# Performance work log

Hardware: AMD Instinct MI355X
Metric: run time of the kernel (lower is better)

Reference implementation:

```python
import jax, jax.numpy as jnp
import numpy as np

N, S, F, E, H, O, L, FE = 8, 1024, 64, 512, 8, 64, 6, 4
HD = E // H
FF = FE * E


def setup_inputs() -> dict:
    key = jax.random.key(0)
    ks = iter(jax.random.split(key, 40))
    def rn(shape, s=0.02):
        return jax.random.normal(next(ks), shape, jnp.float32) * s
    return {
        'x': jax.random.normal(next(ks), (N, F, S), jnp.float32),
        'W_first': rn((F, E)), 'b_first': jnp.zeros((E,), jnp.float32),
        'pos_emb': rn((S, E)),
        'Wq': rn((L, HD, HD)), 'bq': jnp.zeros((L, HD), jnp.float32),
        'Wk': rn((L, HD, HD)), 'bk': jnp.zeros((L, HD), jnp.float32),
        'Wv': rn((L, HD, HD)), 'bv': jnp.zeros((L, HD), jnp.float32),
        'Wo': rn((L, E, E)), 'bo': jnp.zeros((L, E), jnp.float32),
        'g1': jnp.ones((L, E), jnp.float32), 'be1': jnp.zeros((L, E), jnp.float32),
        'Wf1': rn((L, E, FF)), 'bf1': jnp.zeros((L, FF), jnp.float32),
        'Wf2': rn((L, FF, E)), 'bf2': jnp.zeros((L, E), jnp.float32),
        'g2': jnp.ones((L, E), jnp.float32), 'be2': jnp.zeros((L, E), jnp.float32),
        'Wfin': rn((E, O)), 'bfin': jnp.zeros((O,), jnp.float32),
    }


def layernorm(x, g, b, eps=1e-5):
    m = jnp.mean(x, axis=-1, keepdims=True)
    v = jnp.mean(jnp.square(x - m), axis=-1, keepdims=True)
    return (x - m) * jax.lax.rsqrt(v + eps) * g + b


def reference(x, W_first, b_first, pos_emb, Wq, bq, Wk, bk, Wv, bv, Wo, bo,
              g1, be1, Wf1, bf1, Wf2, bf2, g2, be2, Wfin, bfin):
    # x: (N, F, S) -> (N, S, F)
    h = jax.nn.relu(jnp.einsum('nfs,fe->nse', x, W_first) + b_first) + pos_emb[None]
    scale = E ** 0.5  # note: module scales by sqrt(embed_size), not sqrt(head_dim)
    for i in range(L):
        t = h.reshape(N, S, H, HD)
        q = jnp.einsum('nshd,de->nshe', t, Wq[i]) + bq[i]
        k = jnp.einsum('nshd,de->nshe', t, Wk[i]) + bk[i]
        v = jnp.einsum('nshd,de->nshe', t, Wv[i]) + bv[i]
        energy = jnp.einsum('nqhd,nkhd->nhqk', q, k)  # (N,H,S,S)
        att = jax.nn.softmax(energy / scale, axis=-1)
        o = jnp.einsum('nhqk,nkhd->nqhd', att, v).reshape(N, S, E)
        o = jnp.einsum('nse,ef->nsf', o, Wo[i]) + bo[i]
        hx = layernorm(o + h, g1[i], be1[i])
        ff = jax.nn.relu(jnp.einsum('nse,ef->nsf', hx, Wf1[i]) + bf1[i])
        ff = jnp.einsum('nsf,fe->nse', ff, Wf2[i]) + bf2[i]
        h = layernorm(ff + hx, g2[i], be2[i])
    # Conv1d kernel_size=1 == pointwise linear over channels; output (N, O, S)
    return jnp.einsum('nse,eo->nos', h, Wfin) + bfin[None, :, None]
```

## Files before the change

kernel.cpp:

```cpp
#include <hip/hip_runtime.h>
#include <hip/hip_bf16.h>
#include <math.h>

#define N_ 8
#define S_ 1024
#define F_ 64
#define E_ 512
#define H_ 8
#define O_ 64
#define L_ 6
#define HD_ 64
#define FF_ 2048
#define SCALE_ 0.044194173824159216f
#define LOG2E_ 1.4426950408889634f
#define QSCALE_ (SCALE_ * LOG2E_)

typedef unsigned short u16;
typedef __attribute__((ext_vector_type(4))) unsigned short u16x4;
typedef __attribute__((ext_vector_type(8))) unsigned short u16x8;
typedef __attribute__((ext_vector_type(8))) short short8;
typedef __attribute__((ext_vector_type(4))) float floatx4;

__device__ __forceinline__ u16 f2b(float f) {
    union { float f; unsigned u; } v; v.f = f;
    unsigned u = v.u;
    unsigned r = (u + 0x7FFFu + ((u >> 16) & 1u)) >> 16;
    return (u16)r;
}
__device__ __forceinline__ u16 f2b_fast(float f) {
    union { float f; unsigned u; } v; v.f = f;
    return (u16)((v.u + 0x8000u) >> 16);
}
__device__ __forceinline__ float b2f(u16 h) {
    union { unsigned u; float f; } v; v.u = ((unsigned)h) << 16;
    return v.f;
}

__device__ __forceinline__ void gload16(const u16* g, u16* l) {
    __builtin_amdgcn_global_load_lds(
        (const __attribute__((address_space(1))) void*)g,
        (__attribute__((address_space(3))) void*)l, 16, 0, 0);
}

__global__ __launch_bounds__(256) void first_mfma(
    const float* __restrict__ x, const u16* __restrict__ wt,
    const float* __restrict__ bf, const float* __restrict__ pe,
    u16* __restrict__ resb)
{
    __shared__ u16 a_s[128][72];
    int t = threadIdx.x;
    int w = t >> 6, lane = t & 63, quad = lane >> 4, c16 = lane & 15;
    int rowhalf = w >> 1, colhalf = w & 1;
    int col0 = blockIdx.x * 128;
    int row0 = blockIdx.y * 128;
    int n = row0 >> 10, s0 = row0 & 1023;

    const float* xb = x + (size_t)n * F_ * S_ + s0;
    #pragma unroll
    for (int i = 0; i < 8; i++) {
        int pos = (t + i * 256) * 4;
        int f = pos >> 7, sl = pos & 127;
        float4 v = *(const float4*)&xb[(size_t)f * S_ + sl];
        a_s[sl + 0][f] = f2b_fast(v.x);
        a_s[sl + 1][f] = f2b_fast(v.y);
        a_s[sl + 2][f] = f2b_fast(v.z);
        a_s[sl + 3][f] = f2b_fast(v.w);
    }
    __syncthreads();

    floatx4 acc[4][4];
    #pragma unroll
    for (int mt = 0; mt < 4; mt++)
        #pragma unroll
        for (int nt = 0; nt < 4; nt++) acc[mt][nt] = (floatx4){0.f, 0.f, 0.f, 0.f};

    #pragma unroll
    for (int ks = 0; ks < 2; ks++) {
        short8 af[4], bfr[4];
        #pragma unroll
        for (int mt = 0; mt < 4; mt++)
            af[mt] = *(const short8*)&a_s[rowhalf * 64 + mt * 16 + c16][ks * 32 + quad * 8];
        #pragma unroll
        for (int nt = 0; nt < 4; nt++)
            bfr[nt] = *(const short8*)&wt[(size_t)(col0 + colhalf * 64 + nt * 16 + c16) * F_
                                          + ks * 32 + quad * 8];
        #pragma unroll
        for (int mt = 0; mt < 4; mt++)
            #pragma unroll
            for (int nt = 0; nt < 4; nt++)
                acc[mt][nt] = __builtin_amdgcn_mfma_f32_16x16x32_bf16(
                    af[mt], bfr[nt], acc[mt][nt], 0, 0, 0);
    }

    #pragma unroll
    for (int nt = 0; nt < 4; nt++) {
        int col = col0 + colhalf * 64 + nt * 16 + c16;
        float bv = bf[col];
        #pragma unroll
        for (int mt = 0; mt < 4; mt++) {
            #pragma unroll
            for (int r = 0; r < 4; r++) {
                size_t row = (size_t)row0 + rowhalf * 64 + mt * 16 + quad * 4 + r;
                int s = (int)(row & 1023);
                float v = fmaxf(acc[mt][nt][r] + bv, 0.f) + pe[(size_t)s * E_ + col];
                resb[row * E_ + col] = f2b_fast(v);
            }
        }
    }
}

__global__ __launch_bounds__(256) void wprep(
    const float* __restrict__ W_first, const float* __restrict__ Wo,
    const float* __restrict__ Wf1, const float* __restrict__ Wf2,
    const float* __restrict__ Wfin,
    const float* __restrict__ Wq, const float* __restrict__ Wk,
    const float* __restrict__ Wv,
    u16* __restrict__ w1t, u16* __restrict__ wot, u16* __restrict__ wf1t,
    u16* __restrict__ wf2t, u16* __restrict__ wft,
    u16* __restrict__ wqt, u16* __restrict__ wkt, u16* __restrict__ wvt)
{
    int b = blockIdx.x;
    int t = threadIdx.x;
    __shared__ float tile[32][33];
    const float* W; u16* Wt; int K, Nc, bx, by;
    if (b < 32) {
        W = W_first; Wt = w1t; K = F_; Nc = E_; bx = b & 15; by = b >> 4;
    } else if (b < 32 + 1536) {
        int i = b - 32; int z = i >> 8; int r = i & 255;
        W = Wo + (size_t)z * E_ * E_; Wt = wot + (size_t)z * E_ * E_;
        K = E_; Nc = E_; bx = r & 15; by = r >> 4;
    } else if (b < 32 + 1536 + 6144) {
        int i = b - (32 + 1536); int z = i >> 10; int r = i & 1023;
        W = Wf1 + (size_t)z * E_ * FF_; Wt = wf1t + (size_t)z * E_ * FF_;
        K = E_; Nc = FF_; bx = r & 63; by = r >> 6;
    } else if (b < 32 + 1536 + 12288) {
        int i = b - (32 + 1536 + 6144); int z = i >> 10; int r = i & 1023;
        W = Wf2 + (size_t)z * FF_ * E_; Wt = wf2t + (size_t)z * FF_ * E_;
        K = FF_; Nc = E_; bx = r & 15; by = r >> 4;
    } else if (b < 32 + 1536 + 12288 + 32) {
        int r = b - (32 + 1536 + 12288);
        W = Wfin; Wt = wft; K = E_; Nc = O_; bx = r & 1; by = r >> 1;
    } else {
        int l = b - (32 + 1536 + 12288 + 32);
        size_t off = (size_t)l * HD_ * HD_;
        #pragma unroll
        for (int i = 0; i < 16; i++) {
            int idx = t + i * 256;
            int e = idx >> 6, d = idx & 63;
            wqt[off + idx] = f2b(Wq[off + d * HD_ + e]);
            wkt[off + idx] = f2b(Wk[off + d * HD_ + e]);
            wvt[off + idx] = f2b(Wv[off + d * HD_ + e]);
        }
        return;
    }
    #pragma unroll
    for (int i = 0; i < 4; i++) {
        int q = t + i * 256; int r = q >> 5, c = q & 31;
        tile[r][c] = W[(size_t)(by * 32 + r) * Nc + bx * 32 + c];
    }
    __syncthreads();
    #pragma unroll
    for (int i = 0; i < 4; i++) {
        int q = t + i * 256; int r = q >> 5, c = q & 31;
        Wt[(size_t)(bx * 32 + r) * K + by * 32 + c] = f2b(tile[c][r]);
    }
}

__global__ __launch_bounds__(256) void qkv_mfma(
    const u16* __restrict__ hb,
    const u16* __restrict__ wqt, const u16* __restrict__ wkt,
    const u16* __restrict__ wvt,
    const float* __restrict__ bq, const float* __restrict__ bk,
    const float* __restrict__ bvp,
    u16* __restrict__ qo, u16* __restrict__ ko, u16* __restrict__ vt)
{
    __shared__ u16 a_s[128 * 64];
    int t = threadIdx.x;
    int w = t >> 6, lane = t & 63, quad = lane >> 4, c16 = lane & 15;
    size_t row0 = (size_t)blockIdx.x * 128;

    #pragma unroll
    for (int i = 0; i < 4; i++) {
        int q = t + i * 256; int r = q >> 3, c = q & 7;
        *(u16x8*)&a_s[r * 64 + ((c ^ (r & 7)) * 8)] =
            *(const u16x8*)&hb[(row0 + r) * HD_ + c * 8];
    }
    __syncthreads();

    short8 af[2][2];
    #pragma unroll
    for (int mt = 0; mt < 2; mt++)
        #pragma unroll
        for (int ks = 0; ks < 2; ks++) {
            int r = w * 32 + mt * 16 + c16;
            af[mt][ks] = *(const short8*)&a_s[r * 64 + (((ks * 4 + quad) ^ (r & 7)) * 8)];
        }

    const u16* wts[2] = {wqt, wkt};
    const float* bs[2] = {bq, bk};
    u16* outs[2] = {qo, ko};
    #pragma unroll
    for (int m = 0; m < 2; m++) {
        short8 bfr[4][2];
        #pragma unroll
        for (int nt = 0; nt < 4; nt++)
            #pragma unroll
            for (int ks = 0; ks < 2; ks++)
                bfr[nt][ks] = *(const short8*)&wts[m][(nt * 16 + c16) * HD_ + ks * 32 + quad * 8];
        floatx4 acc[2][4];
        #pragma unroll
        for (int mt = 0; mt < 2; mt++)
            #pragma unroll
            for (int nt = 0; nt < 4; nt++) acc[mt][nt] = (floatx4){0.f, 0.f, 0.f, 0.f};
        #pragma unroll
        for (int ks = 0; ks < 2; ks++)
            #pragma unroll
            for (int mt = 0; mt < 2; mt++)
                #pragma unroll
                for (int nt = 0; nt < 4; nt++)
                    acc[mt][nt] = __builtin_amdgcn_mfma_f32_16x16x32_bf16(
                        af[mt][ks], bfr[nt][ks], acc[mt][nt], 0, 0, 0);
        float osc = (m == 0) ? QSCALE_ : 1.0f;
        #pragma unroll
        for (int nt = 0; nt < 4; nt++) {
            float bv_ = bs[m][nt * 16 + c16];
            #pragma unroll
            for (int mt = 0; mt < 2; mt++)
                #pragma unroll
                for (int r = 0; r < 4; r++)
                    outs[m][(row0 + w * 32 + mt * 16 + quad * 4 + r) * HD_ + nt * 16 + c16] =
                        f2b_fast((acc[mt][nt][r] + bv_) * osc);
        }
    }

    {
        short8 bfr[4][2];
        #pragma unroll
        for (int nt = 0; nt < 4; nt++)
            #pragma unroll
            for (int ks = 0; ks < 2; ks++)
                bfr[nt][ks] = *(const short8*)&wvt[(nt * 16 + c16) * HD_ + ks * 32 + quad * 8];
        floatx4 acc[2][4];
        #pragma unroll
        for (int mt = 0; mt < 2; mt++)
            #pragma unroll
            for (int nt = 0; nt < 4; nt++) acc[mt][nt] = (floatx4){0.f, 0.f, 0.f, 0.f};
        #pragma unroll
        for (int ks = 0; ks < 2; ks++)
            #pragma unroll
            for (int mt = 0; mt < 2; mt++)
                #pragma unroll
                for (int nt = 0; nt < 4; nt++)
                    acc[mt][nt] = __builtin_amdgcn_mfma_f32_16x16x32_bf16(
                        af[mt][ks], bfr[nt][ks], acc[mt][nt], 0, 0, 0);

        __syncthreads();
        u16* vt_s = a_s;
        #pragma unroll
        for (int nt = 0; nt < 4; nt++) {
            float bv_ = bvp[nt * 16 + c16];
            #pragma unroll
            for (int mt = 0; mt < 2; mt++)
                #pragma unroll
                for (int r = 0; r < 4; r++) {
                    int fr = w * 32 + mt * 16 + quad * 4 + r;
                    int h = fr & 7, sl = fr >> 3;
                    vt_s[((h * 64 + nt * 16 + c16) * 16) + sl] =
                        f2b_fast(acc[mt][nt][r] + bv_);
                }
        }
        __syncthreads();
        int sflat0 = (int)(row0 >> 3);
        int n = sflat0 >> 10, sbase = sflat0 & 1023;
        #pragma unroll
        for (int i = 0; i < 4; i++) {
            int u = t + i * 256;
            int h = u >> 7, rest = u & 127, d = rest >> 1, half = rest & 1;
            *(u16x8*)&vt[((size_t)((n * 8 + h) * 64 + d)) * (size_t)S_ + sbase + half * 8] =
                *(u16x8*)&vt_s[(h * 64 + d) * 16 + half * 8];
        }
    }
}

__global__ __launch_bounds__(256, 4) void attn_mfma(
    const u16* __restrict__ Q, const u16* __restrict__ K,
    const u16* __restrict__ Vt, u16* __restrict__ O)
{
    int bid0 = blockIdx.x;
    int bid = (bid0 & 7) * 128 + (bid0 >> 3);
    int qt = bid & 15, hh = (bid >> 4) & 7, n = bid >> 7;
    int t = threadIdx.x;
    int w = t >> 6, lane = t & 63, quad = lane >> 4, c16 = lane & 15;

    __shared__ u16 qp_s[64 * 64];
    __shared__ u16 k_s[2][64 * 64];
    __shared__ u16 vt_s[2][64 * 64];
    u16* p_s = qp_s + w * 16 * 64;

    const size_t qkbase = (size_t)n * S_ * E_ + hh * 64;
    const size_t vtbase = ((size_t)(n * H_ + hh) * 64) * (size_t)S_;

    int ar = t >> 3, act = t & 7;
    int acq = act * 8;
    int scw[2];
    #pragma unroll
    for (int i = 0; i < 2; i++) scw[i] = ((act ^ ((ar + i * 32) & 7)) * 8);

    #pragma unroll
    for (int i = 0; i < 2; i++) {
        int q = t + i * 256; int r = q >> 3, c = q & 7;
        *(u16x8*)&qp_s[r * 64 + ((c ^ (r & 7)) * 8)] =
            *(const u16x8*)&Q[qkbase + (size_t)(qt * 64 + r) * E_ + c * 8];
    }
    u16x8 pk[2], pv[2];
    #pragma unroll
    for (int i = 0; i < 2; i++) {
        pk[i] = *(const u16x8*)&K[qkbase + (size_t)(ar + i * 32) * E_ + acq];
        pv[i] = *(const u16x8*)&Vt[vtbase + (size_t)(ar + i * 32) * S_ + acq];
    }
    __syncthreads();

    short8 qf[2];
    #pragma unroll
    for (int ks = 0; ks < 2; ks++) {
        int r = w * 16 + c16;
        qf[ks] = *(const short8*)&qp_s[r * 64 + (((ks * 4 + quad) ^ (r & 7)) * 8)];
    }

    #pragma unroll
    for (int i = 0; i < 2; i++) {
        int r = ar + i * 32;
        *(u16x8*)&k_s[0][r * 64 + scw[i]] = pk[i];
        *(u16x8*)&vt_s[0][r * 64 + scw[i]] = pv[i];
    }
    __syncthreads();

    const short8 ones = {(short)0x3F80, (short)0x3F80, (short)0x3F80, (short)0x3F80,
                         (short)0x3F80, (short)0x3F80, (short)0x3F80, (short)0x3F80};

    floatx4 oaccT[4];
    floatx4 lacc = (floatx4){0.f, 0.f, 0.f, 0.f};
    #pragma unroll
    for (int mt = 0; mt < 4; mt++) oaccT[mt] = (floatx4){0.f, 0.f, 0.f, 0.f};

    for (int k0 = 0; k0 < S_; k0 += 64) {
        int cur = (k0 >> 6) & 1;
        const u16* ks_ = k_s[cur];
        const u16* vs_ = vt_s[cur];
        bool more = (k0 + 64 < S_);
        if (more) {
            #pragma unroll
            for (int i = 0; i < 2; i++) {
                pk[i] = *(const u16x8*)&K[qkbase + (size_t)(k0 + 64 + ar + i * 32) * E_ + acq];
                pv[i] = *(const u16x8*)&Vt[vtbase + (size_t)(ar + i * 32) * S_ + k0 + 64 + acq];
            }
        }

        floatx4 st[4];
        #pragma unroll
        for (int mt = 0; mt < 4; mt++) st[mt] = (floatx4){0.f, 0.f, 0.f, 0.f};
        __builtin_amdgcn_s_setprio(1);
        #pragma unroll
        for (int ks = 0; ks < 2; ks++) {
            short8 kf[4];
            #pragma unroll
            for (int mt = 0; mt < 4; mt++) {
                int r = mt * 16 + c16;
                kf[mt] = *(const short8*)&ks_[r * 64 + (((ks * 4 + quad) ^ (r & 7)) * 8)];
            }
            #pragma unroll
            for (int mt = 0; mt < 4; mt++)
                st[mt] = __builtin_amdgcn_mfma_f32_16x16x32_bf16(
                    kf[mt], qf[ks], st[mt], 0, 0, 0);
        }
        __builtin_amdgcn_s_setprio(0);

        #pragma unroll
        for (int mt = 0; mt < 4; mt++) {
            u16x4 h;
            #pragma unroll
            for (int r = 0; r < 4; r++) h[r] = f2b_fast(exp2f(st[mt][r]));
            *(u16x4*)&p_s[c16 * 64 + (((2 * mt + (quad >> 1)) ^ (c16 & 7)) * 8)
                          + (quad & 1) * 4] = h;
        }

        __builtin_amdgcn_s_setprio(1);
        #pragma unroll
        for (int ks = 0; ks < 2; ks++) {
            short8 pf = *(const short8*)&p_s[c16 * 64 + (((ks * 4 + quad) ^ (c16 & 7)) * 8)];
            short8 vf[4];
            #pragma unroll
            for (int mt = 0; mt < 4; mt++) {
                int r = mt * 16 + c16;
                vf[mt] = *(const short8*)&vs_[r * 64 + (((ks * 4 + quad) ^ (r & 7)) * 8)];
            }
            lacc = __builtin_amdgcn_mfma_f32_16x16x32_bf16(ones, pf, lacc, 0, 0, 0);
            #pragma unroll
            for (int mt = 0; mt < 4; mt++)
                oaccT[mt] = __builtin_amdgcn_mfma_f32_16x16x32_bf16(
                    vf[mt], pf, oaccT[mt], 0, 0, 0);
        }
        __builtin_amdgcn_s_setprio(0);

        if (more) {
            u16* kd = k_s[cur ^ 1];
            u16* vd = vt_s[cur ^ 1];
            #pragma unroll
            for (int i = 0; i < 2; i++) {
                int r = ar + i * 32;
                *(u16x8*)&kd[r * 64 + scw[i]] = pk[i];
                *(u16x8*)&vd[r * 64 + scw[i]] = pv[i];
            }
        }
        __syncthreads();
    }

    {
        float rl = 1.f / lacc[0];
        int s = qt * 64 + w * 16 + c16;
        size_t base = (size_t)(n * S_ + s) * E_ + hh * 64;
        #pragma unroll
        for (int mt = 0; mt < 4; mt++) {
            u16x4 h;
            #pragma unroll
            for (int r = 0; r < 4; r++) h[r] = f2b_fast(oaccT[mt][r] * rl);
            *(u16x4*)&O[base + mt * 16 + quad * 4] = h;
        }
    }
}

template <int MT, int NT, bool RELU, bool HASRES, bool OUTF32, bool OUTBF16>
__global__ __launch_bounds__(256, 2) void gemm_mfma(
    const u16* __restrict__ A, const u16* __restrict__ Bt,
    const float* __restrict__ bias, const u16* __restrict__ resid,
    float* __restrict__ outf, u16* __restrict__ outb, int M, int Nc, int K)
{
    constexpr int MFR = MT / 32;
    constexpr int NFR = NT / 32;
    constexpr int AI  = MT / 32;
    constexpr int BI  = NT / 32;
    __shared__ u16 a_s[MT * 64];
    __shared__ u16 b_s[NT * 64];

    int t = threadIdx.x;
    int w = t >> 6, lane = t & 63, quad = lane >> 4, c16 = lane & 15;
    int rw = w >> 1, cw = w & 1;

    int gx = gridDim.x;
    int nwg = gx * (int)gridDim.y;
    int lin = (int)blockIdx.y * gx + (int)blockIdx.x;
    int cpx = nwg >> 3;
    int id2 = (lin & 7) * cpx + (lin >> 3);
    int bx = id2 % gx, by = id2 / gx;

    size_t row0 = (size_t)by * MT;
    size_t col0 = (size_t)bx * NT;

    size_t aoff[AI]; int adst[AI];
    #pragma unroll
    for (int i = 0; i < AI; i++) {
        int p = t + i * 256;
        int r = p >> 3;
        int kc = (p & 7) ^ (r & 7);
        aoff[i] = (row0 + r) * (size_t)K + kc * 8;
        adst[i] = w * 512 + i * 2048;
    }
    size_t boff[BI]; int bdst[BI];
    #pragma unroll
    for (int i = 0; i < BI; i++) {
        int p = t + i * 256;
        int r = p >> 3;
        int kc = (p & 7) ^ (r & 7);
        boff[i] = (col0 + r) * (size_t)K + kc * 8;
        bdst[i] = w * 512 + i * 2048;
    }

    floatx4 acc[MFR][NFR];
    #pragma unroll
    for (int mt = 0; mt < MFR; mt++)
        #pragma unroll
        for (int nt = 0; nt < NFR; nt++) acc[mt][nt] = (floatx4){0.f, 0.f, 0.f, 0.f};

    for (int k0 = 0; k0 < K; k0 += 64) {
        #pragma unroll
        for (int i = 0; i < AI; i++) gload16(A + aoff[i] + k0, a_s + adst[i]);
        #pragma unroll
        for (int i = 0; i < BI; i++) gload16(Bt + boff[i] + k0, b_s + bdst[i]);
        __syncthreads();

        #pragma unroll
        for (int ks = 0; ks < 2; ks++) {
            short8 af[MFR], bfr[NFR];
            #pragma unroll
            for (int mt = 0; mt < MFR; mt++) {
                int r = rw * (MT / 2) + mt * 16 + c16;
                af[mt] = *(const short8*)&a_s[r * 64 + (((ks * 4 + quad) ^ (r & 7)) * 8)];
            }
            #pragma unroll
            for (int nt = 0; nt < NFR; nt++) {
                int r = cw * (NT / 2) + nt * 16 + c16;
                bfr[nt] = *(const short8*)&b_s[r * 64 + (((ks * 4 + quad) ^ (r & 7)) * 8)];
            }
            #pragma unroll
            for (int mt = 0; mt < MFR; mt++)
                #pragma unroll
                for (int nt = 0; nt < NFR; nt++)
                    acc[mt][nt] = __builtin_amdgcn_mfma_f32_16x16x32_bf16(
                        af[mt], bfr[nt], acc[mt][nt], 0, 0, 0);
        }
        __syncthreads();
    }

    #pragma unroll
    for (int nt = 0; nt < NFR; nt++) {
        int col = (int)col0 + cw * (NT / 2) + nt * 16 + c16;
        float bv = bias[col];
        #pragma unroll
        for (int mt = 0; mt < MFR; mt++) {
            size_t rowb = row0 + rw * (MT / 2) + mt * 16 + quad * 4;
            #pragma unroll
            for (int r = 0; r < 4; r++) {
                size_t row = rowb + r;
                float v = acc[mt][nt][r] + bv;
                if constexpr (HASRES) v += b2f(resid[row * Nc + col]);
                if constexpr (RELU) v = fmaxf(v, 0.f);
                if constexpr (OUTF32) outf[row * Nc + col] = v;
                if constexpr (OUTBF16) outb[row * Nc + col] = f2b_fast(v);
            }
        }
    }
}

__global__ __launch_bounds__(256) void layernorm_k(
    const float* __restrict__ in, const float* __restrict__ g,
    const float* __restrict__ bb, u16* __restrict__ outb)
{
    int row = blockIdx.x;
    int t = threadIdx.x;
    const float* x = in + (size_t)row * E_;
    float x0 = x[t], x1 = x[t + 256];
    float s = x0 + x1;
    #pragma unroll
    for (int off = 32; off; off >>= 1) s += __shfl_down(s, off, 64);
    __shared__ float red[4];
    int wid = t >> 6, lane = t & 63;
    if (lane == 0) red[wid] = s;
    __syncthreads();
    float m = (red[0] + red[1] + red[2] + red[3]) * (1.f / E_);
    float d0 = x0 - m, d1 = x1 - m;
    float sq = d0 * d0 + d1 * d1;
    #pragma unroll
    for (int off = 32; off; off >>= 1) sq += __shfl_down(sq, off, 64);
    __syncthreads();
    if (lane == 0) red[wid] = sq;
    __syncthreads();
    float var = (red[0] + red[1] + red[2] + red[3]) * (1.f / E_);
    float rstd = rsqrtf(var + 1e-5f);
    outb[(size_t)row * E_ + t] = f2b_fast(d0 * rstd * g[t] + bb[t]);
    outb[(size_t)row * E_ + t + 256] = f2b_fast(d1 * rstd * g[t + 256] + bb[t + 256]);
}

__global__ __launch_bounds__(256) void final_mfma(
    const u16* __restrict__ hb, const u16* __restrict__ wft,
    const float* __restrict__ bfin, float* __restrict__ outp)
{
    __shared__ u16 a_s[64][72];
    int t = threadIdx.x;
    int w = t >> 6, lane = t & 63, quad = lane >> 4, c16 = lane & 15;
    size_t row0 = (size_t)blockIdx.x * 64;

    floatx4 acc[4];
    #pragma unroll
    for (int nt = 0; nt < 4; nt++) acc[nt] = (floatx4){0.f, 0.f, 0.f, 0.f};

    int ar = t >> 3, acq = (t & 7) * 8;
    u16x8 pa[2];
    #pragma unroll
    for (int i = 0; i < 2; i++)
        pa[i] = *(const u16x8*)&hb[(row0 + ar + i * 32) * E_ + acq];

    for (int k0 = 0; k0 < E_; k0 += 64) {
        #pragma unroll
        for (int i = 0; i < 2; i++)
            *(u16x8*)&a_s[ar + i * 32][acq] = pa[i];
        __syncthreads();
        if (k0 + 64 < E_) {
            #pragma unroll
            for (int i = 0; i < 2; i++)
                pa[i] = *(const u16x8*)&hb[(row0 + ar + i * 32) * E_ + k0 + 64 + acq];
        }
        #pragma unroll
        for (int ks = 0; ks < 2; ks++) {
            short8 af = *(const short8*)&a_s[w * 16 + c16][ks * 32 + quad * 8];
            #pragma unroll
            for (int nt = 0; nt < 4; nt++) {
                short8 bf = *(const short8*)&wft[(nt * 16 + c16) * E_ + k0 + ks * 32 + quad * 8];
                acc[nt] = __builtin_amdgcn_mfma_f32_16x16x32_bf16(af, bf, acc[nt], 0, 0, 0);
            }
        }
        __syncthreads();
    }

    #pragma unroll
    for (int nt = 0; nt < 4; nt++) {
        int o = nt * 16 + c16;
        float bv = bfin[o];
        #pragma unroll
        for (int r = 0; r < 4; r++) {
            size_t row = row0 + w * 16 + quad * 4 + r;
            int n = (int)(row >> 10), s = (int)(row & 1023);
            outp[((size_t)(n * O_ + o)) * S_ + s] = acc[nt][r] + bv;
        }
    }
}

extern "C" void kernel_launch(void* const* d_in, const int* in_sizes, int n_in,
                              void* d_out, int out_size, void* d_ws, size_t ws_size,
                              hipStream_t stream)
{
    const float* x       = (const float*)d_in[0];
    const float* W_first = (const float*)d_in[1];
    const float* b_first = (const float*)d_in[2];
    const float* pos_emb = (const float*)d_in[3];
    const float* Wq      = (const float*)d_in[4];
    const float* bq      = (const float*)d_in[5];
    const float* Wk      = (const float*)d_in[6];
    const float* bk      = (const float*)d_in[7];
    const float* Wv      = (const float*)d_in[8];
    const float* bv      = (const float*)d_in[9];
    const float* Wo      = (const float*)d_in[10];
    const float* bo      = (const float*)d_in[11];
    const float* g1      = (const float*)d_in[12];
    const float* be1     = (const float*)d_in[13];
    const float* Wf1     = (const float*)d_in[14];
    const float* bf1     = (const float*)d_in[15];
    const float* Wf2     = (const float*)d_in[16];
    const float* bf2     = (const float*)d_in[17];
    const float* g2      = (const float*)d_in[18];
    const float* be2     = (const float*)d_in[19];
    const float* Wfin    = (const float*)d_in[20];
    const float* bfin    = (const float*)d_in[21];
    float* out = (float*)d_out;

    const size_t M4 = (size_t)N_ * S_ * E_;
    float* t1   = (float*)d_ws;
    u16*   resb = (u16*)(t1 + M4);
    u16*   qb   = resb + M4;
    u16*   kb   = qb + M4;
    u16*   vt   = kb + M4;
    u16*   ob   = vt + M4;
    u16*   ffb  = qb;
    u16*   wot  = ob + M4;
    u16*   wf1t = wot + (size_t)L_ * E_ * E_;
    u16*   wf2t = wf1t + (size_t)L_ * E_ * FF_;
    u16*   wqt  = wf2t + (size_t)L_ * FF_ * E_;
    u16*   wkt  = wqt + (size_t)L_ * HD_ * HD_;
    u16*   wvt  = wkt + (size_t)L_ * HD_ * HD_;
    u16*   wft  = wvt + (size_t)L_ * HD_ * HD_;
    u16*   w1t  = wft + (size_t)O_ * E_;

    const int rows = N_ * S_;

    wprep<<<32 + 1536 + 12288 + 32 + 6, 256, 0, stream>>>(
        W_first, Wo, Wf1, Wf2, Wfin, Wq, Wk, Wv,
        w1t, wot, wf1t, wf2t, wft, wqt, wkt, wvt);

    first_mfma<<<dim3(E_ / 128, rows / 128), 256, 0, stream>>>(
        x, w1t, b_first, pos_emb, resb);

    for (int i = 0; i < L_; i++) {
        qkv_mfma<<<512, 256, 0, stream>>>(
            resb, wqt + (size_t)i * HD_ * HD_, wkt + (size_t)i * HD_ * HD_,
            wvt + (size_t)i * HD_ * HD_, bq + i * HD_, bk + i * HD_, bv + i * HD_,
            qb, kb, vt);
        attn_mfma<<<1024, 256, 0, stream>>>(qb, kb, vt, ob);
        gemm_mfma<128, 64, false, true, true, false><<<dim3(E_ / 64, rows / 128), 256, 0, stream>>>(
            ob, wot + (size_t)i * E_ * E_, bo + i * E_, resb, t1, nullptr, rows, E_, E_);
        layernorm_k<<<rows, 256, 0, stream>>>(t1, g1 + i * E_, be1 + i * E_, resb);
        gemm_mfma<128, 128, true, false, false, true><<<dim3(FF_ / 128, rows / 128), 256, 0, stream>>>(
            resb, wf1t + (size_t)i * E_ * FF_, bf1 + i * FF_, nullptr, nullptr, ffb,
            rows, FF_, E_);
        gemm_mfma<128, 64, false, true, true, false><<<dim3(E_ / 64, rows / 128), 256, 0, stream>>>(
            ffb, wf2t + (size_t)i * FF_ * E_, bf2 + i * E_, resb, t1, nullptr,
            rows, E_, FF_);
        layernorm_k<<<rows, 256, 0, stream>>>(t1, g2 + i * E_, be2 + i * E_, resb);
    }

    final_mfma<<<rows / 64, 256, 0, stream>>>(resb, wft, bfin, out);
}
```

Measured before the change: 1.005 ms.

## Load attention K/V and QKV inputs directly from global memory, dropping LDS staging

The attention kernel no longer stages K and V^T tiles in double-buffered shared memory. Each wave now loads its MFMA fragments straight from global memory (through cache) every iteration, which removes the block-wide barriers and LDS traffic. The QKV projection kernel likewise reads its A fragments from global memory instead of going through LDS. The trade is that every one of the four waves re-reads the same K/V tile from L2, the loads are no longer prefetched ahead of use, and global access patterns become less coalesced. That exposes memory latency inside the loop.

```diff
diff --git a/kernel.cpp b/kernel.cpp
--- a/kernel.cpp
+++ b/kernel.cpp
@@ -174,27 +174,18 @@
     const float* __restrict__ bvp,
     u16* __restrict__ qo, u16* __restrict__ ko, u16* __restrict__ vt)
 {
-    __shared__ u16 a_s[128 * 64];
+    __shared__ u16 vt_s[128 * 64];
     int t = threadIdx.x;
     int w = t >> 6, lane = t & 63, quad = lane >> 4, c16 = lane & 15;
     size_t row0 = (size_t)blockIdx.x * 128;
 
-    #pragma unroll
-    for (int i = 0; i < 4; i++) {
-        int q = t + i * 256; int r = q >> 3, c = q & 7;
-        *(u16x8*)&a_s[r * 64 + ((c ^ (r & 7)) * 8)] =
-            *(const u16x8*)&hb[(row0 + r) * HD_ + c * 8];
-    }
-    __syncthreads();
-
     short8 af[2][2];
     #pragma unroll
     for (int mt = 0; mt < 2; mt++)
         #pragma unroll
-        for (int ks = 0; ks < 2; ks++) {
-            int r = w * 32 + mt * 16 + c16;
-            af[mt][ks] = *(const short8*)&a_s[r * 64 + (((ks * 4 + quad) ^ (r & 7)) * 8)];
-        }
+        for (int ks = 0; ks < 2; ks++)
+            af[mt][ks] = *(const short8*)&hb[(row0 + w * 32 + mt * 16 + c16) * HD_
+                                             + ks * 32 + quad * 8];
 
     const u16* wts[2] = {wqt, wkt};
     const float* bs[2] = {bq, bk};
@@ -254,8 +245,6 @@
                     acc[mt][nt] = __builtin_amdgcn_mfma_f32_16x16x32_bf16(
                         af[mt][ks], bfr[nt][ks], acc[mt][nt], 0, 0, 0);
 
-        __syncthreads();
-        u16* vt_s = a_s;
         #pragma unroll
         for (int nt = 0; nt < 4; nt++) {
             float bv_ = bvp[nt * 16 + c16];
@@ -292,48 +281,20 @@
     int t = threadIdx.x;
     int w = t >> 6, lane = t & 63, quad = lane >> 4, c16 = lane & 15;
 
-    __shared__ u16 qp_s[64 * 64];
-    __shared__ u16 k_s[2][64 * 64];
-    __shared__ u16 vt_s[2][64 * 64];
-    u16* p_s = qp_s + w * 16 * 64;
+    __shared__ u16 p_all[4 * 16 * 64];
+    u16* p_s = p_all + w * 16 * 64;
 
     const size_t qkbase = (size_t)n * S_ * E_ + hh * 64;
     const size_t vtbase = ((size_t)(n * H_ + hh) * 64) * (size_t)S_;
 
-    int ar = t >> 3, act = t & 7;
-    int acq = act * 8;
-    int scw[2];
-    #pragma unroll
-    for (int i = 0; i < 2; i++) scw[i] = ((act ^ ((ar + i * 32) & 7)) * 8);
-
-    #pragma unroll
-    for (int i = 0; i < 2; i++) {
-        int q = t + i * 256; int r = q >> 3, c = q & 7;
-        *(u16x8*)&qp_s[r * 64 + ((c ^ (r & 7)) * 8)] =
-            *(const u16x8*)&Q[qkbase + (size_t)(qt * 64 + r) * E_ + c * 8];
-    }
-    u16x8 pk[2], pv[2];
-    #pragma unroll
-    for (int i = 0; i < 2; i++) {
-        pk[i] = *(const u16x8*)&K[qkbase + (size_t)(ar + i * 32) * E_ + acq];
-        pv[i] = *(const u16x8*)&Vt[vtbase + (size_t)(ar + i * 32) * S_ + acq];
-    }
-    __syncthreads();
-
     short8 qf[2];
     #pragma unroll
-    for (int ks = 0; ks < 2; ks++) {
-        int r = w * 16 + c16;
-        qf[ks] = *(const short8*)&qp_s[r * 64 + (((ks * 4 + quad) ^ (r & 7)) * 8)];
-    }
-
-    #pragma unroll
-    for (int i = 0; i < 2; i++) {
-        int r = ar + i * 32;
-        *(u16x8*)&k_s[0][r * 64 + scw[i]] = pk[i];
-        *(u16x8*)&vt_s[0][r * 64 + scw[i]] = pv[i];
-    }
-    __syncthreads();
+    for (int ks = 0; ks < 2; ks++)
+        qf[ks] = *(const short8*)&Q[qkbase + (size_t)(qt * 64 + w * 16 + c16) * E_
+                                    + ks * 32 + quad * 8];
+
+    const u16* kp = K + qkbase + (size_t)c16 * E_ + quad * 8;
+    const u16* vp = Vt + vtbase + (size_t)c16 * S_ + quad * 8;
 
     const short8 ones = {(short)0x3F80, (short)0x3F80, (short)0x3F80, (short)0x3F80,
                          (short)0x3F80, (short)0x3F80, (short)0x3F80, (short)0x3F80};
@@ -344,36 +305,31 @@
     for (int mt = 0; mt < 4; mt++) oaccT[mt] = (floatx4){0.f, 0.f, 0.f, 0.f};
 
     for (int k0 = 0; k0 < S_; k0 += 64) {
-        int cur = (k0 >> 6) & 1;
-        const u16* ks_ = k_s[cur];
-        const u16* vs_ = vt_s[cur];
-        bool more = (k0 + 64 < S_);
-        if (more) {
-            #pragma unroll
-            for (int i = 0; i < 2; i++) {
-                pk[i] = *(const u16x8*)&K[qkbase + (size_t)(k0 + 64 + ar + i * 32) * E_ + acq];
-                pv[i] = *(const u16x8*)&Vt[vtbase + (size_t)(ar + i * 32) * S_ + k0 + 64 + acq];
-            }
-        }
+        short8 kf[2][4];
+        #pragma unroll
+        for (int ks = 0; ks < 2; ks++)
+            #pragma unroll
+            for (int mt = 0; mt < 4; mt++)
+                kf[ks][mt] = *(const short8*)&kp[(size_t)(k0 + mt * 16) * E_ + ks * 32];
 
         floatx4 st[4];
         #pragma unroll
         for (int mt = 0; mt < 4; mt++) st[mt] = (floatx4){0.f, 0.f, 0.f, 0.f};
         __builtin_amdgcn_s_setprio(1);
         #pragma unroll
-        for (int ks = 0; ks < 2; ks++) {
-            short8 kf[4];
-            #pragma unroll
-            for (int mt = 0; mt < 4; mt++) {
-                int r = mt * 16 + c16;
-                kf[mt] = *(const short8*)&ks_[r * 64 + (((ks * 4 + quad) ^ (r & 7)) * 8)];
-            }
+        for (int ks = 0; ks < 2; ks++)
             #pragma unroll
             for (int mt = 0; mt < 4; mt++)
                 st[mt] = __builtin_amdgcn_mfma_f32_16x16x32_bf16(
-                    kf[mt], qf[ks], st[mt], 0, 0, 0);
-        }
+                    kf[ks][mt], qf[ks], st[mt], 0, 0, 0);
         __builtin_amdgcn_s_setprio(0);
+
+        short8 vf[2][4];
+        #pragma unroll
+        for (int ks = 0; ks < 2; ks++)
+            #pragma unroll
+            for (int mt = 0; mt < 4; mt++)
+                vf[ks][mt] = *(const short8*)&vp[(size_t)(mt * 16) * S_ + k0 + ks * 32];
 
         #pragma unroll
         for (int mt = 0; mt < 4; mt++) {
@@ -388,31 +344,13 @@
         #pragma unroll
         for (int ks = 0; ks < 2; ks++) {
             short8 pf = *(const short8*)&p_s[c16 * 64 + (((ks * 4 + quad) ^ (c16 & 7)) * 8)];
-            short8 vf[4];
-            #pragma unroll
-            for (int mt = 0; mt < 4; mt++) {
-                int r = mt * 16 + c16;
-                vf[mt] = *(const short8*)&vs_[r * 64 + (((ks * 4 + quad) ^ (r & 7)) * 8)];
-            }
             lacc = __builtin_amdgcn_mfma_f32_16x16x32_bf16(ones, pf, lacc, 0, 0, 0);
             #pragma unroll
             for (int mt = 0; mt < 4; mt++)
                 oaccT[mt] = __builtin_amdgcn_mfma_f32_16x16x32_bf16(
-                    vf[mt], pf, oaccT[mt], 0, 0, 0);
+                    vf[ks][mt], pf, oaccT[mt], 0, 0, 0);
         }
         __builtin_amdgcn_s_setprio(0);
-
-        if (more) {
-            u16* kd = k_s[cur ^ 1];
-            u16* vd = vt_s[cur ^ 1];
-            #pragma unroll
-            for (int i = 0; i < 2; i++) {
-                int r = ar + i * 32;
-                *(u16x8*)&kd[r * 64 + scw[i]] = pk[i];
-                *(u16x8*)&vd[r * 64 + scw[i]] = pv[i];
-            }
-        }
-        __syncthreads();
     }
 
     {
```

Measured after the change: 1.461 ms. 45.4% more time.

## Double query tile per attention block, load QKV A-fragments directly, vectorize layernorm

Applied to the files above, without the earlier changes.

Attention blocks now cover 128 queries instead of 64, with each wave holding two 16-row query fragments. Every K/V tile loaded into shared memory is therefore reused across twice as many queries, and the grid is halved. The cost is more accumulator registers, so occupancy drops to 2 blocks per SM. The QKV kernel now reads A-fragments straight from global memory, skipping the LDS staging and one barrier, and layernorm uses float2 loads and packed bf16 stores.

```diff
diff --git a/kernel.cpp b/kernel.cpp
--- a/kernel.cpp
+++ b/kernel.cpp
@@ -174,27 +174,18 @@
     const float* __restrict__ bvp,
     u16* __restrict__ qo, u16* __restrict__ ko, u16* __restrict__ vt)
 {
-    __shared__ u16 a_s[128 * 64];
+    __shared__ u16 vt_s[128 * 64];
     int t = threadIdx.x;
     int w = t >> 6, lane = t & 63, quad = lane >> 4, c16 = lane & 15;
     size_t row0 = (size_t)blockIdx.x * 128;
 
-    #pragma unroll
-    for (int i = 0; i < 4; i++) {
-        int q = t + i * 256; int r = q >> 3, c = q & 7;
-        *(u16x8*)&a_s[r * 64 + ((c ^ (r & 7)) * 8)] =
-            *(const u16x8*)&hb[(row0 + r) * HD_ + c * 8];
-    }
-    __syncthreads();
-
     short8 af[2][2];
     #pragma unroll
     for (int mt = 0; mt < 2; mt++)
         #pragma unroll
-        for (int ks = 0; ks < 2; ks++) {
-            int r = w * 32 + mt * 16 + c16;
-            af[mt][ks] = *(const short8*)&a_s[r * 64 + (((ks * 4 + quad) ^ (r & 7)) * 8)];
-        }
+        for (int ks = 0; ks < 2; ks++)
+            af[mt][ks] = *(const short8*)&hb[(row0 + w * 32 + mt * 16 + c16) * HD_
+                                             + ks * 32 + quad * 8];
 
     const u16* wts[2] = {wqt, wkt};
     const float* bs[2] = {bq, bk};
@@ -254,8 +245,6 @@
                     acc[mt][nt] = __builtin_amdgcn_mfma_f32_16x16x32_bf16(
                         af[mt][ks], bfr[nt][ks], acc[mt][nt], 0, 0, 0);
 
-        __syncthreads();
-        u16* vt_s = a_s;
         #pragma unroll
         for (int nt = 0; nt < 4; nt++) {
             float bv_ = bvp[nt * 16 + c16];
@@ -282,20 +271,20 @@
     }
 }
 
-__global__ __launch_bounds__(256, 4) void attn_mfma(
+__global__ __launch_bounds__(256, 2) void attn_mfma(
     const u16* __restrict__ Q, const u16* __restrict__ K,
     const u16* __restrict__ Vt, u16* __restrict__ O)
 {
     int bid0 = blockIdx.x;
-    int bid = (bid0 & 7) * 128 + (bid0 >> 3);
-    int qt = bid & 15, hh = (bid >> 4) & 7, n = bid >> 7;
+    int bid = (bid0 & 7) * 64 + (bid0 >> 3);
+    int qt = bid & 7, hh = (bid >> 3) & 7, n = bid >> 6;
     int t = threadIdx.x;
     int w = t >> 6, lane = t & 63, quad = lane >> 4, c16 = lane & 15;
 
-    __shared__ u16 qp_s[64 * 64];
+    __shared__ u16 qp_s[128 * 64];
     __shared__ u16 k_s[2][64 * 64];
     __shared__ u16 vt_s[2][64 * 64];
-    u16* p_s = qp_s + w * 16 * 64;
+    u16* p_s = qp_s + w * 32 * 64;
 
     const size_t qkbase = (size_t)n * S_ * E_ + hh * 64;
     const size_t vtbase = ((size_t)(n * H_ + hh) * 64) * (size_t)S_;
@@ -307,10 +296,10 @@
     for (int i = 0; i < 2; i++) scw[i] = ((act ^ ((ar + i * 32) & 7)) * 8);
 
     #pragma unroll
-    for (int i = 0; i < 2; i++) {
+    for (int i = 0; i < 4; i++) {
         int q = t + i * 256; int r = q >> 3, c = q & 7;
         *(u16x8*)&qp_s[r * 64 + ((c ^ (r & 7)) * 8)] =
-            *(const u16x8*)&Q[qkbase + (size_t)(qt * 64 + r) * E_ + c * 8];
+            *(const u16x8*)&Q[qkbase + (size_t)(qt * 128 + r) * E_ + c * 8];
     }
     u16x8 pk[2], pv[2];
     #pragma unroll
@@ -320,12 +309,14 @@
     }
     __syncthreads();
 
-    short8 qf[2];
-    #pragma unroll
-    for (int ks = 0; ks < 2; ks++) {
-        int r = w * 16 + c16;
-        qf[ks] = *(const short8*)&qp_s[r * 64 + (((ks * 4 + quad) ^ (r & 7)) * 8)];
-    }
+    short8 qf[2][2];
+    #pragma unroll
+    for (int nq = 0; nq < 2; nq++)
+        #pragma unroll
+        for (int ks = 0; ks < 2; ks++) {
+            int r = w * 32 + nq * 16 + c16;
+            qf[nq][ks] = *(const short8*)&qp_s[r * 64 + (((ks * 4 + quad) ^ (r & 7)) * 8)];
+        }
 
     #pragma unroll
     for (int i = 0; i < 2; i++) {
@@ -338,10 +329,14 @@
     const short8 ones = {(short)0x3F80, (short)0x3F80, (short)0x3F80, (short)0x3F80,
                          (short)0x3F80, (short)0x3F80, (short)0x3F80, (short)0x3F80};
 
-    floatx4 oaccT[4];
-    floatx4 lacc = (floatx4){0.f, 0.f, 0.f, 0.f};
-    #pragma unroll
-    for (int mt = 0; mt < 4; mt++) oaccT[mt] = (floatx4){0.f, 0.f, 0.f, 0.f};
+    floatx4 oaccT[4][2];
+    floatx4 lacc[2];
+    #pragma unroll
+    for (int nq = 0; nq < 2; nq++) {
+        lacc[nq] = (floatx4){0.f, 0.f, 0.f, 0.f};
+        #pragma unroll
+        for (int mt = 0; mt < 4; mt++) oaccT[mt][nq] = (floatx4){0.f, 0.f, 0.f, 0.f};
+    }
 
     for (int k0 = 0; k0 < S_; k0 += 64) {
         int cur = (k0 >> 6) & 1;
@@ -356,9 +351,11 @@
             }
         }
 
-        floatx4 st[4];
-        #pragma unroll
-        for (int mt = 0; mt < 4; mt++) st[mt] = (floatx4){0.f, 0.f, 0.f, 0.f};
+        floatx4 st[4][2];
+        #pragma unroll
+        for (int mt = 0; mt < 4; mt++)
+            #pragma unroll
+            for (int nq = 0; nq < 2; nq++) st[mt][nq] = (floatx4){0.f, 0.f, 0.f, 0.f};
         __builtin_amdgcn_s_setprio(1);
         #pragma unroll
         for (int ks = 0; ks < 2; ks++) {
@@ -370,35 +367,48 @@
             }
             #pragma unroll
             for (int mt = 0; mt < 4; mt++)
-                st[mt] = __builtin_amdgcn_mfma_f32_16x16x32_bf16(
-                    kf[mt], qf[ks], st[mt], 0, 0, 0);
+                #pragma unroll
+                for (int nq = 0; nq < 2; nq++)
+                    st[mt][nq] = __builtin_amdgcn_mfma_f32_16x16x32_bf16(
+                        kf[mt], qf[nq][ks], st[mt][nq], 0, 0, 0);
         }
         __builtin_amdgcn_s_setprio(0);
 
         #pragma unroll
-        for (int mt = 0; mt < 4; mt++) {
-            u16x4 h;
-            #pragma unroll
-            for (int r = 0; r < 4; r++) h[r] = f2b_fast(exp2f(st[mt][r]));
-            *(u16x4*)&p_s[c16 * 64 + (((2 * mt + (quad >> 1)) ^ (c16 & 7)) * 8)
-                          + (quad & 1) * 4] = h;
-        }
+        for (int nq = 0; nq < 2; nq++)
+            #pragma unroll
+            for (int mt = 0; mt < 4; mt++) {
+                u16x4 h;
+                #pragma unroll
+                for (int r = 0; r < 4; r++) h[r] = f2b_fast(exp2f(st[mt][nq][r]));
+                *(u16x4*)&p_s[(nq * 16 + c16) * 64
+                              + (((2 * mt + (quad >> 1)) ^ (c16 & 7)) * 8)
+                              + (quad & 1) * 4] = h;
+            }
 
         __builtin_amdgcn_s_setprio(1);
         #pragma unroll
         for (int ks = 0; ks < 2; ks++) {
-            short8 pf = *(const short8*)&p_s[c16 * 64 + (((ks * 4 + quad) ^ (c16 & 7)) * 8)];
+            short8 pf[2];
+            #pragma unroll
+            for (int nq = 0; nq < 2; nq++) {
+                int r = nq * 16 + c16;
+                pf[nq] = *(const short8*)&p_s[r * 64 + (((ks * 4 + quad) ^ (c16 & 7)) * 8)];
+            }
             short8 vf[4];
             #pragma unroll
             for (int mt = 0; mt < 4; mt++) {
                 int r = mt * 16 + c16;
                 vf[mt] = *(const short8*)&vs_[r * 64 + (((ks * 4 + quad) ^ (r & 7)) * 8)];
             }
-            lacc = __builtin_amdgcn_mfma_f32_16x16x32_bf16(ones, pf, lacc, 0, 0, 0);
-            #pragma unroll
-            for (int mt = 0; mt < 4; mt++)
-                oaccT[mt] = __builtin_amdgcn_mfma_f32_16x16x32_bf16(
-                    vf[mt], pf, oaccT[mt], 0, 0, 0);
+            #pragma unroll
+            for (int nq = 0; nq < 2; nq++) {
+                lacc[nq] = __builtin_amdgcn_mfma_f32_16x16x32_bf16(ones, pf[nq], lacc[nq], 0, 0, 0);
+                #pragma unroll
+                for (int mt = 0; mt < 4; mt++)
+                    oaccT[mt][nq] = __builtin_amdgcn_mfma_f32_16x16x32_bf16(
+                        vf[mt], pf[nq], oaccT[mt][nq], 0, 0, 0);
+            }
         }
         __builtin_amdgcn_s_setprio(0);
 
@@ -415,15 +425,16 @@
         __syncthreads();
     }
 
-    {
-        float rl = 1.f / lacc[0];
-        int s = qt * 64 + w * 16 + c16;
+    #pragma unroll
+    for (int nq = 0; nq < 2; nq++) {
+        float rl = 1.f / lacc[nq][0];
+        int s = qt * 128 + w * 32 + nq * 16 + c16;
         size_t base = (size_t)(n * S_ + s) * E_ + hh * 64;
         #pragma unroll
         for (int mt = 0; mt < 4; mt++) {
             u16x4 h;
             #pragma unroll
-            for (int r = 0; r < 4; r++) h[r] = f2b_fast(oaccT[mt][r] * rl);
+            for (int r = 0; r < 4; r++) h[r] = f2b_fast(oaccT[mt][nq][r] * rl);
             *(u16x4*)&O[base + mt * 16 + quad * 4] = h;
         }
     }
@@ -538,8 +549,8 @@
     int row = blockIdx.x;
     int t = threadIdx.x;
     const float* x = in + (size_t)row * E_;
-    float x0 = x[t], x1 = x[t + 256];
-    float s = x0 + x1;
+    float2 xv = *(const float2*)&x[t * 2];
+    float s = xv.x + xv.y;
     #pragma unroll
     for (int off = 32; off; off >>= 1) s += __shfl_down(s, off, 64);
     __shared__ float red[4];
@@ -547,7 +558,7 @@
     if (lane == 0) red[wid] = s;
     __syncthreads();
     float m = (red[0] + red[1] + red[2] + red[3]) * (1.f / E_);
-    float d0 = x0 - m, d1 = x1 - m;
+    float d0 = xv.x - m, d1 = xv.y - m;
     float sq = d0 * d0 + d1 * d1;
     #pragma unroll
     for (int off = 32; off; off >>= 1) sq += __shfl_down(sq, off, 64);
@@ -556,8 +567,11 @@
     __syncthreads();
     float var = (red[0] + red[1] + red[2] + red[3]) * (1.f / E_);
     float rstd = rsqrtf(var + 1e-5f);
-    outb[(size_t)row * E_ + t] = f2b_fast(d0 * rstd * g[t] + bb[t]);
-    outb[(size_t)row * E_ + t + 256] = f2b_fast(d1 * rstd * g[t + 256] + bb[t + 256]);
+    float2 gv = *(const float2*)&g[t * 2];
+    float2 bv = *(const float2*)&bb[t * 2];
+    unsigned o = (unsigned)f2b_fast(d0 * rstd * gv.x + bv.x)
+               | ((unsigned)f2b_fast(d1 * rstd * gv.y + bv.y) << 16);
+    *(unsigned*)&outb[(size_t)row * E_ + t * 2] = o;
 }
 
 __global__ __launch_bounds__(256) void final_mfma(
@@ -673,7 +687,7 @@
             resb, wqt + (size_t)i * HD_ * HD_, wkt + (size_t)i * HD_ * HD_,
             wvt + (size_t)i * HD_ * HD_, bq + i * HD_, bk + i * HD_, bv + i * HD_,
             qb, kb, vt);
-        attn_mfma<<<1024, 256, 0, stream>>>(qb, kb, vt, ob);
+        attn_mfma<<<512, 256, 0, stream>>>(qb, kb, vt, ob);
         gemm_mfma<128, 64, false, true, true, false><<<dim3(E_ / 64, rows / 128), 256, 0, stream>>>(
             ob, wot + (size_t)i * E_ * E_, bo + i * E_, resb, t1, nullptr, rows, E_, E_);
         layernorm_k<<<rows, 256, 0, stream>>>(t1, g1 + i * E_, be1 + i * E_, resb);
```

New measurement: 991.3 us. About the same (-1.3%).
